# Kernel tuning notes

Measured on AMD Instinct MI355X. Metric: run time of the kernel, lower is better.

Reference implementation:

```python
import jax, jax.numpy as jnp
import numpy as np

B, L, D, E, K = 8, 384, 1024, 4, 2
H = 4 * D  # expert MLP hidden


def setup_inputs() -> dict:
    key = jax.random.key(0)
    ks = jax.random.split(key, 10)
    def w(k, shape, fan_in):
        return jax.random.normal(k, shape, jnp.float32) / np.sqrt(fan_in).astype(np.float32)
    return {
        "context_c": jax.random.normal(ks[0], (B, L, D), jnp.float32),
        "time_cond": jax.random.normal(ks[1], (B, D), jnp.float32),
        "gate_W": w(ks[2], (E, 3 * D), 3 * D),
        "gate_b": jnp.zeros((E,), jnp.float32),
        "tmod_W": w(ks[3], (2 * E, D), D),
        "tmod_b": jnp.zeros((2 * E,), jnp.float32),
        "eW1": w(ks[4], (E, D, H), D),
        "eb1": jnp.zeros((E, H), jnp.float32),
        "eW2": w(ks[5], (E, H, D), H),
        "eb2": jnp.zeros((E, D), jnp.float32),
        "sW1": w(ks[6], (D, H), D),
        "sb1": jnp.zeros((H,), jnp.float32),
        "sW2": w(ks[7], (H, D), H),
        "sb2": jnp.zeros((D,), jnp.float32),
    }


def reference(context_c, time_cond, gate_W, gate_b, tmod_W, tmod_b,
              eW1, eb1, eW2, eb2, sW1, sb1, sW2, sb2):
    Lh = Lw = L // 3
    Lp = L - Lh - Lw
    head = context_c[:, :Lh]            # (B, Lh, D)
    wrist = context_c[:, Lh:Lh + Lw]    # (B, Lw, D)
    prop = context_c[:, Lh + Lw:]       # (B, Lp, D)

    # per-sample modality-combo aggregates for the gate
    full_agg = context_c.mean(axis=1)
    hp_agg = (head.sum(axis=1) + prop.sum(axis=1)) / (Lh + Lp)
    wp_agg = (wrist.sum(axis=1) + prop.sum(axis=1)) / (Lw + Lp)
    gate_in = jnp.concatenate([full_agg, hp_agg, wp_agg], axis=-1)  # (B, 3D)

    logits = gate_in @ gate_W.T + gate_b                            # (B, E)
    mod = jax.nn.silu(time_cond) @ tmod_W.T + tmod_b                # (B, 2E)
    scale, shift = mod[:, :E], mod[:, E:]
    logits = logits * (1.0 + scale) + shift

    scores = jax.nn.softmax(logits, axis=-1)
    tw, ti = jax.lax.top_k(scores, K)                               # (B, K)
    tw = tw / (tw.sum(axis=-1, keepdims=True) + 1e-8)
    # per-sample combined weight for each expert: (B, E)
    w_be = (jax.nn.one_hot(ti, E, dtype=tw.dtype) * tw[..., None]).sum(axis=1)

    # modality mask per expert (E, L): expert 1 skips wrist, expert 2 skips head
    mask_np = np.ones((E, L), np.float32)
    mask_np[1, Lh:Lh + Lw] = 0.0
    mask_np[2, :Lh] = 0.0
    mask = jnp.asarray(mask_np)

    # run all experts on all tokens (token-wise MLP), combine with per-sample
    # routing weights and per-expert modality masks — identical math to the
    # original per-sample sliced dispatch.
    h = jax.nn.gelu(jnp.einsum('bld,edh->belh', context_c, eW1)
                    + eb1[None, :, None, :], approximate=True)      # (B,E,L,H)
    y = jnp.einsum('belh,ehd->beld', h, eW2) + eb2[None, :, None, :]
    out = jnp.einsum('be,el,beld->bld', w_be, mask, y)

    # shared expert (always-on)
    shared = jax.nn.gelu(context_c @ sW1 + sb1, approximate=True) @ sW2 + sb2
    return out + shared
```

## Files before the change

### kernel.cpp

```cpp
#include <hip/hip_runtime.h>
#include <cstdint>
#include <cstddef>


#define DEV __device__ __forceinline__

typedef __attribute__((ext_vector_type(8))) __bf16 bf16x8;
typedef __attribute__((ext_vector_type(4))) __bf16 bf16x4;
typedef __attribute__((ext_vector_type(4))) float f32x4;

static constexpr int Bb = 8, Ll = 384, Dd = 1024, Ee = 4, Hh = 4096;

DEV void load_lds16(const void* g, void* l) {
  __builtin_amdgcn_global_load_lds(
      (const __attribute__((address_space(1))) void*)g,
      (__attribute__((address_space(3))) void*)l, 16, 0, 0);
}

DEV float gelu_tanh(float x) {
  float u = 0.7978845608028654f * (x + 0.044715f * x * x * x);
  float t = 1.0f - 2.0f / (1.0f + __expf(2.0f * u));
  return 0.5f * x * (1.0f + t);
}

DEV float wave_red(float v) {
#pragma unroll
  for (int o = 32; o > 0; o >>= 1) v += __shfl_down(v, o, 64);
  return v;
}


__global__ void cvt_x_kernel(const float* __restrict__ src, __bf16* __restrict__ dst, int n4) {
  int i = blockIdx.x * blockDim.x + threadIdx.x;
  if (i >= n4) return;
  float4 v = ((const float4*)src)[i];
  bf16x4 o;
  o.x = (__bf16)v.x; o.y = (__bf16)v.y; o.z = (__bf16)v.z; o.w = (__bf16)v.w;
  ((bf16x4*)dst)[i] = o;
}

__global__ void transpose_cvt_kernel(const float* __restrict__ src, __bf16* __restrict__ dst,
                                     int nr, int nc) {
  __shared__ float t[32][33];
  size_t base = (size_t)blockIdx.z * nr * nc;
  src += base; dst += base;
  int x = threadIdx.x & 31, y = threadIdx.x >> 5;
  int c0 = blockIdx.x * 32, r0 = blockIdx.y * 32;
#pragma unroll
  for (int r = 0; r < 4; ++r) {
    int rr = y + r * 8;
    t[rr][x] = src[(size_t)(r0 + rr) * nc + c0 + x];
  }
  __syncthreads();
#pragma unroll
  for (int r = 0; r < 4; ++r) {
    int rr = y + r * 8;
    dst[(size_t)(c0 + rr) * nr + r0 + x] = (__bf16)t[x][rr];
  }
}


__global__ void agg_kernel(const float* __restrict__ ctx, float* __restrict__ part) {
  int c = blockIdx.x, b = blockIdx.y, t = threadIdx.x;
  int d0 = t * 4;
  float4 sum = {0.f, 0.f, 0.f, 0.f};
  const float* p = ctx + ((size_t)(b * Ll + c * 64)) * Dd + d0;
  for (int l = 0; l < 64; ++l) {
    float4 v = *(const float4*)(p + (size_t)l * Dd);
    sum.x += v.x; sum.y += v.y; sum.z += v.z; sum.w += v.w;
  }
  *(float4*)(part + ((size_t)(b * 6 + c)) * Dd + d0) = sum;
}

__global__ void gate_kernel(const float* __restrict__ part, const float* __restrict__ tc,
                            const float* __restrict__ gW, const float* __restrict__ gb,
                            const float* __restrict__ tW, const float* __restrict__ tb,
                            int* __restrict__ slotE, float* __restrict__ slotW) {
  __shared__ float gi[3 * Dd];
  __shared__ float st[Dd];
  __shared__ float red[12];
  int b = blockIdx.x, t = threadIdx.x;
  const float* pb = part + (size_t)b * 6 * Dd;
#pragma unroll
  for (int k = 0; k < 4; ++k) {
    int d = t * 4 + k;
    float p0 = pb[d], p1 = pb[Dd + d], p2 = pb[2 * Dd + d];
    float p3 = pb[3 * Dd + d], p4 = pb[4 * Dd + d], p5 = pb[5 * Dd + d];
    gi[d]          = (p0 + p1 + p2 + p3 + p4 + p5) * (1.0f / 384.0f);
    gi[Dd + d]     = (p0 + p1 + p4 + p5) * (1.0f / 256.0f);
    gi[2 * Dd + d] = (p2 + p3 + p4 + p5) * (1.0f / 256.0f);
    float tv = tc[b * Dd + d];
    st[d] = tv / (1.0f + __expf(-tv));
  }
  __syncthreads();
  int wid = t >> 6, lane = t & 63;
  float aL = 0.f;
  for (int i = lane; i < 3 * Dd; i += 64) aL += gi[i] * gW[wid * 3 * Dd + i];
  aL = wave_red(aL);
  float aA = 0.f, aB = 0.f;
  for (int i = lane; i < Dd; i += 64) {
    float s = st[i];
    aA += s * tW[wid * Dd + i];
    aB += s * tW[(wid + 4) * Dd + i];
  }
  aA = wave_red(aA); aB = wave_red(aB);
  if (lane == 0) { red[wid] = aL; red[4 + wid] = aA; red[8 + wid] = aB; }
  __syncthreads();
  if (t == 0) {
    float lg[4];
#pragma unroll
    for (int e = 0; e < 4; ++e) {
      float logit = red[e] + gb[e];
      float scale = red[4 + e] + tb[e];
      float shift = red[8 + e] + tb[4 + e];
      lg[e] = logit * (1.0f + scale) + shift;
    }
    float m = fmaxf(fmaxf(lg[0], lg[1]), fmaxf(lg[2], lg[3]));
    float p[4], sum = 0.f;
#pragma unroll
    for (int e = 0; e < 4; ++e) { p[e] = __expf(lg[e] - m); sum += p[e]; }
#pragma unroll
    for (int e = 0; e < 4; ++e) p[e] /= sum;
    int i0 = 0;
    for (int e = 1; e < 4; ++e) if (p[e] > p[i0]) i0 = e;
    int i1 = -1;
    for (int e = 0; e < 4; ++e) if (e != i0 && (i1 < 0 || p[e] > p[i1])) i1 = e;
    float sw = p[i0] + p[i1] + 1e-8f;
    slotE[b * 4 + 0] = i0; slotE[b * 4 + 1] = i1;
    slotW[b * 4 + 0] = p[i0] / sw; slotW[b * 4 + 1] = p[i1] / sw;
  }
}


__global__ __launch_bounds__(256) void gemm1_kernel(
    const __bf16* __restrict__ Xbf, const __bf16* __restrict__ W1T,
    const __bf16* __restrict__ S1T, const float* __restrict__ eb1,
    const float* __restrict__ sb1, const int* __restrict__ slotE,
    const float* __restrict__ slotW, __bf16* __restrict__ Hbuf, int bbase) {
  constexpr int K = Dd;
  int nt = blockIdx.x, mt = blockIdx.y, z = blockIdx.z;
  int bl = z / 3, s = z - bl * 3;
  int b = bbase + bl;
  int e = (s == 2) ? Ee : slotE[b * 4 + s];
  if ((e == 1 && mt == 1) || (e == 2 && mt == 0)) return;
  float wgt = (s == 2) ? 1.0f : slotW[b * 4 + s];

  const __bf16* Ab = Xbf + ((size_t)(b * Ll + mt * 128)) * K;
  const __bf16* Bbp = (e < Ee ? W1T + (size_t)e * Hh * K : S1T) + (size_t)(nt * 128) * K;
  const float* b1p = (e < Ee ? eb1 + e * Hh : sb1);

  __shared__ __align__(16) char smem[65536];

  int tid = threadIdx.x, wid = tid >> 6, lane = tid & 63;
  int q = lane >> 4, l16 = lane & 15;
  int wm = wid >> 1, wn = wid & 1;

  const __bf16* gp[8];
  uint32_t lo[8];
#pragma unroll
  for (int u = 0; u < 8; ++u) {
    int c = wid * 8 + u;
    int isB = c >> 4;
    int blk = (c & 15) >> 1;
    int ks = c & 1;
    const __bf16* base = isB ? Bbp : Ab;
    gp[u] = base + (size_t)(blk * 16 + l16) * K + ks * 32 + q * 8;
    lo[u] = (uint32_t)(isB * 16384 + (blk * 2 + ks) * 1024);
  }

  f32x4 acc[4][4];
  f32x4 zero = {0.f, 0.f, 0.f, 0.f};
#pragma unroll
  for (int i = 0; i < 4; ++i)
#pragma unroll
    for (int j = 0; j < 4; ++j) acc[i][j] = zero;

#pragma unroll
  for (int u = 0; u < 8; ++u) load_lds16(gp[u], smem + lo[u]);

  constexpr int NK = K / 64;
  for (int kt = 0; kt < NK; ++kt) {
    int ph = kt & 1;
    __syncthreads();
    if (kt + 1 < NK) {
#pragma unroll
      for (int u = 0; u < 8; ++u) {
        gp[u] += 64;
        load_lds16(gp[u], smem + lo[u] + (ph ^ 1) * 32768);
      }
    }
    const char* sm = (const char*)smem + ph * 32768;
#pragma unroll
    for (int ks = 0; ks < 2; ++ks) {
      bf16x8 a[4], bb[4];
#pragma unroll
      for (int i = 0; i < 4; ++i)
        a[i] = *(const bf16x8*)(sm + (((wm * 4 + i) * 2 + ks) * 64 + lane) * 16);
#pragma unroll
      for (int j = 0; j < 4; ++j)
        bb[j] = *(const bf16x8*)(sm + 16384 + (((wn * 4 + j) * 2 + ks) * 64 + lane) * 16);
#pragma unroll
      for (int i = 0; i < 4; ++i)
#pragma unroll
        for (int j = 0; j < 4; ++j)
          acc[i][j] = __builtin_amdgcn_mfma_f32_16x16x32_bf16(a[i], bb[j], acc[i][j], 0, 0, 0);
    }
  }

  float bias[4];
#pragma unroll
  for (int j = 0; j < 4; ++j) bias[j] = b1p[nt * 128 + wn * 64 + j * 16 + l16];

  __syncthreads();
  __bf16* tile = (__bf16*)smem;
#pragma unroll
  for (int i = 0; i < 4; ++i)
#pragma unroll
    for (int j = 0; j < 4; ++j)
#pragma unroll
      for (int r = 0; r < 4; ++r) {
        float x = acc[i][j][r] + bias[j];
        int row = wm * 64 + i * 16 + q * 4 + r;
        int col = wn * 64 + j * 16 + l16;
        tile[row * 136 + col] = (__bf16)(wgt * gelu_tanh(x));
      }
  __syncthreads();
  __bf16* Hrow = Hbuf + ((size_t)(bl * 3 + s) * Ll + mt * 128) * Hh + nt * 128;
#pragma unroll
  for (int t2 = 0; t2 < 8; ++t2) {
    int gidx = t2 * 256 + tid;
    int row = gidx >> 4, cg = gidx & 15;
    bf16x8 v = *(const bf16x8*)(tile + row * 136 + cg * 8);
    *(bf16x8*)(Hrow + (size_t)row * Hh + cg * 8) = v;
  }
}


__global__ __launch_bounds__(256) void gemm2_kernel(
    const __bf16* __restrict__ Hbuf, const __bf16* __restrict__ W2T,
    const __bf16* __restrict__ S2T, const float* __restrict__ eb2,
    const float* __restrict__ sb2, const int* __restrict__ slotE,
    const float* __restrict__ slotW, float* __restrict__ out,
    __bf16* __restrict__ pbuf, int bbase, int bc) {
  constexpr int K = Hh;
  constexpr int KC = 1024;
  int nt = blockIdx.x, mt = blockIdx.y, z = blockIdx.z;
  int kc = z & 3, bl = z >> 2;
  int b = bbase + bl;

  __shared__ __align__(16) char smem[65536];

  int tid = threadIdx.x, wid = tid >> 6, lane = tid & 63;
  int q = lane >> 4, l16 = lane & 15;
  int wm = wid >> 1, wn = wid & 1;

  f32x4 acc[4][4];
  f32x4 zero = {0.f, 0.f, 0.f, 0.f};
#pragma unroll
  for (int i = 0; i < 4; ++i)
#pragma unroll
    for (int j = 0; j < 4; ++j) acc[i][j] = zero;
  float biasacc[4] = {0.f, 0.f, 0.f, 0.f};

  for (int s = 0; s < 3; ++s) {
    int e = (s == 2) ? Ee : slotE[b * 4 + s];
    if ((e == 1 && mt == 1) || (e == 2 && mt == 0)) continue;
    float wgt = (s == 2) ? 1.0f : slotW[b * 4 + s];

    const __bf16* Ab = Hbuf + ((size_t)(bl * 3 + s) * Ll + mt * 128) * K + (size_t)kc * KC;
    const __bf16* Bbp = (e < Ee ? W2T + (size_t)e * Dd * K : S2T) + (size_t)(nt * 128) * K + (size_t)kc * KC;

    const __bf16* gp[8];
    uint32_t lo[8];
#pragma unroll
    for (int u = 0; u < 8; ++u) {
      int c = wid * 8 + u;
      int isB = c >> 4;
      int blk = (c & 15) >> 1;
      int ks = c & 1;
      const __bf16* base = isB ? Bbp : Ab;
      gp[u] = base + (size_t)(blk * 16 + l16) * K + ks * 32 + q * 8;
      lo[u] = (uint32_t)(isB * 16384 + (blk * 2 + ks) * 1024);
    }

#pragma unroll
    for (int u = 0; u < 8; ++u) load_lds16(gp[u], smem + lo[u]);

    constexpr int NK = KC / 64;
    for (int kt = 0; kt < NK; ++kt) {
      int ph = kt & 1;
      __syncthreads();
      if (kt + 1 < NK) {
#pragma unroll
        for (int u = 0; u < 8; ++u) {
          gp[u] += 64;
          load_lds16(gp[u], smem + lo[u] + (ph ^ 1) * 32768);
        }
      }
      const char* sm = (const char*)smem + ph * 32768;
#pragma unroll
      for (int ks = 0; ks < 2; ++ks) {
        bf16x8 a[4], bb[4];
#pragma unroll
        for (int i = 0; i < 4; ++i)
          a[i] = *(const bf16x8*)(sm + (((wm * 4 + i) * 2 + ks) * 64 + lane) * 16);
#pragma unroll
        for (int j = 0; j < 4; ++j)
          bb[j] = *(const bf16x8*)(sm + 16384 + (((wn * 4 + j) * 2 + ks) * 64 + lane) * 16);
#pragma unroll
        for (int i = 0; i < 4; ++i)
#pragma unroll
          for (int j = 0; j < 4; ++j)
            acc[i][j] = __builtin_amdgcn_mfma_f32_16x16x32_bf16(a[i], bb[j], acc[i][j], 0, 0, 0);
      }
    }

    if (kc == 0) {
      const float* b2p = (e < Ee ? eb2 + e * Dd : sb2);
#pragma unroll
      for (int j = 0; j < 4; ++j)
        biasacc[j] += wgt * b2p[nt * 128 + wn * 64 + j * 16 + l16];
    }
  }

  if (pbuf) {
    __syncthreads();
    __bf16* tile = (__bf16*)smem;
#pragma unroll
    for (int i = 0; i < 4; ++i)
#pragma unroll
      for (int j = 0; j < 4; ++j)
#pragma unroll
        for (int r = 0; r < 4; ++r) {
          int row = wm * 64 + i * 16 + q * 4 + r;
          int col = wn * 64 + j * 16 + l16;
          tile[row * 136 + col] = (__bf16)(acc[i][j][r] + biasacc[j]);
        }
    __syncthreads();
    __bf16* Prow = pbuf + (((size_t)(kc * bc + bl) * Ll + mt * 128)) * Dd + nt * 128;
#pragma unroll
    for (int t2 = 0; t2 < 8; ++t2) {
      int gidx = t2 * 256 + tid;
      int row = gidx >> 4, cg = gidx & 15;
      bf16x8 v = *(const bf16x8*)(tile + row * 136 + cg * 8);
      *(bf16x8*)(Prow + (size_t)row * Dd + cg * 8) = v;
    }
  } else {
    float* orow = out + ((size_t)(b * Ll + mt * 128)) * Dd + nt * 128;
#pragma unroll
    for (int i = 0; i < 4; ++i)
#pragma unroll
      for (int j = 0; j < 4; ++j)
#pragma unroll
        for (int r = 0; r < 4; ++r) {
          int row = wm * 64 + i * 16 + q * 4 + r;
          int col = wn * 64 + j * 16 + l16;
          atomicAdd(orow + (size_t)row * Dd + col, acc[i][j][r] + biasacc[j]);
        }
  }
}

__global__ void reduce4_kernel(const __bf16* __restrict__ pbuf, float* __restrict__ out,
                               int n8, size_t stride) {
  int i = blockIdx.x * blockDim.x + threadIdx.x;
  if (i >= n8) return;
  size_t base = (size_t)i * 8;
  float sum[8];
#pragma unroll
  for (int k = 0; k < 8; ++k) sum[k] = 0.f;
#pragma unroll
  for (int kc = 0; kc < 4; ++kc) {
    bf16x8 v = *(const bf16x8*)(pbuf + kc * stride + base);
#pragma unroll
    for (int k = 0; k < 8; ++k) sum[k] += (float)v[k];
  }
  float4 o0 = {sum[0], sum[1], sum[2], sum[3]};
  float4 o1 = {sum[4], sum[5], sum[6], sum[7]};
  *(float4*)(out + base) = o0;
  *(float4*)(out + base + 4) = o1;
}


extern "C" void kernel_launch(void* const* d_in, const int* in_sizes, int n_in,
                              void* d_out, int out_size, void* d_ws, size_t ws_size,
                              hipStream_t stream) {
  (void)in_sizes; (void)n_in;
  const float* ctx = (const float*)d_in[0];
  const float* tc  = (const float*)d_in[1];
  const float* gW  = (const float*)d_in[2];
  const float* gb  = (const float*)d_in[3];
  const float* tW  = (const float*)d_in[4];
  const float* tb  = (const float*)d_in[5];
  const float* eW1 = (const float*)d_in[6];
  const float* eb1 = (const float*)d_in[7];
  const float* eW2 = (const float*)d_in[8];
  const float* eb2 = (const float*)d_in[9];
  const float* sW1 = (const float*)d_in[10];
  const float* sb1 = (const float*)d_in[11];
  const float* sW2 = (const float*)d_in[12];
  const float* sb2 = (const float*)d_in[13];
  float* out = (float*)d_out;

  char* ws = (char*)d_ws;
  size_t off = 0;
  auto alloc = [&](size_t sz) { size_t o = off; off += (sz + 255) & ~(size_t)255; return o; };
  size_t oW1T = alloc((size_t)Ee * Hh * Dd * 2);
  size_t oW2T = alloc((size_t)Ee * Dd * Hh * 2);
  size_t oS1T = alloc((size_t)Hh * Dd * 2);
  size_t oS2T = alloc((size_t)Dd * Hh * 2);
  size_t oX   = alloc((size_t)Bb * Ll * Dd * 2);
  size_t oP   = alloc((size_t)Bb * 6 * Dd * 4);
  size_t oSE  = alloc(Bb * 4 * sizeof(int));
  size_t oSW  = alloc(Bb * 4 * sizeof(float));
  size_t fixed = off;

  auto hbufB = [&](int bc) { return (size_t)bc * 3 * Ll * Hh * 2; };
  auto pbufB = [&](int bc) { return (size_t)4 * bc * Ll * Dd * 2; };
  int bc = 1; bool use_pbuf = false;
  if (fixed + hbufB(8) + pbufB(8) + 512 <= ws_size)      { bc = 8; use_pbuf = true; }
  else if (fixed + hbufB(4) + pbufB(4) + 512 <= ws_size) { bc = 4; use_pbuf = true; }
  else if (fixed + hbufB(4) + 512 <= ws_size)            { bc = 4; use_pbuf = false; }
  else if (fixed + hbufB(2) + 512 <= ws_size)            { bc = 2; use_pbuf = false; }
  else                                                   { bc = 1; use_pbuf = false; }
  int nchunk = Bb / bc;
  size_t oH = alloc(hbufB(bc));
  size_t oPB = use_pbuf ? alloc(pbufB(bc)) : 0;

  __bf16* W1T = (__bf16*)(ws + oW1T);
  __bf16* W2T = (__bf16*)(ws + oW2T);
  __bf16* S1T = (__bf16*)(ws + oS1T);
  __bf16* S2T = (__bf16*)(ws + oS2T);
  __bf16* Xbf = (__bf16*)(ws + oX);
  float*  part = (float*)(ws + oP);
  int*    slotE = (int*)(ws + oSE);
  float*  slotW = (float*)(ws + oSW);
  __bf16* Hbuf = (__bf16*)(ws + oH);
  __bf16* Pbuf = use_pbuf ? (__bf16*)(ws + oPB) : nullptr;

  if (!use_pbuf)
    hipMemsetAsync(d_out, 0, (size_t)out_size * sizeof(float), stream);

  cvt_x_kernel<<<(Bb * Ll * Dd / 4 + 255) / 256, 256, 0, stream>>>(ctx, Xbf, Bb * Ll * Dd / 4);
  transpose_cvt_kernel<<<dim3(Hh / 32, Dd / 32, Ee), 256, 0, stream>>>(eW1, W1T, Dd, Hh);
  transpose_cvt_kernel<<<dim3(Dd / 32, Hh / 32, Ee), 256, 0, stream>>>(eW2, W2T, Hh, Dd);
  transpose_cvt_kernel<<<dim3(Hh / 32, Dd / 32, 1), 256, 0, stream>>>(sW1, S1T, Dd, Hh);
  transpose_cvt_kernel<<<dim3(Dd / 32, Hh / 32, 1), 256, 0, stream>>>(sW2, S2T, Hh, Dd);
  agg_kernel<<<dim3(6, Bb), 256, 0, stream>>>(ctx, part);
  gate_kernel<<<Bb, 256, 0, stream>>>(part, tc, gW, gb, tW, tb, slotE, slotW);

  for (int c = 0; c < nchunk; ++c) {
    gemm1_kernel<<<dim3(Hh / 128, 3, bc * 3), 256, 0, stream>>>(
        Xbf, W1T, S1T, eb1, sb1, slotE, slotW, Hbuf, c * bc);
    gemm2_kernel<<<dim3(Dd / 128, 3, bc * 4), 256, 0, stream>>>(
        Hbuf, W2T, S2T, eb2, sb2, slotE, slotW, out, Pbuf, c * bc, bc);
    if (use_pbuf) {
      int n8 = bc * Ll * Dd / 8;
      reduce4_kernel<<<(n8 + 255) / 256, 256, 0, stream>>>(
          Pbuf, out + (size_t)c * bc * Ll * Dd, n8, (size_t)bc * Ll * Dd);
    }
  }
}
```

Baseline: 581.3 us.

## Remap GEMM workgroups XCD-aware and deepen gemm2 split-K to eight chunks

Both GEMM kernels switch to a flat 1D grid and remap block IDs so consecutive logical tiles land on the same XCD (bid&7 striding). This is meant to improve L2 reuse of weight and activation tiles across the MI355X chiplets. gemm2 is templated on its K-chunk size and, when workspace allows, uses 8 K-chunks of 512 instead of 4 of 1024, doubling the block count to fill more CUs. The cost is a larger partial buffer and more reduction traffic in the generalized reduce kernel.

```diff
diff --git a/kernel.cpp b/kernel.cpp
--- a/kernel.cpp
+++ b/kernel.cpp
@@ -138,8 +138,13 @@
     const float* __restrict__ sb1, const int* __restrict__ slotE,
     const float* __restrict__ slotW, __bf16* __restrict__ Hbuf, int bbase) {
   constexpr int K = Dd;
-  int nt = blockIdx.x, mt = blockIdx.y, z = blockIdx.z;
-  int bl = z / 3, s = z - bl * 3;
+  int bid = blockIdx.x, nwg = gridDim.x;
+  int lid = (bid & 7) * (nwg >> 3) + (bid >> 3);
+  int nt = lid & 31;
+  int r = lid >> 5;
+  int mt = r % 3; r /= 3;
+  int s = r % 3;
+  int bl = r / 3;
   int b = bbase + bl;
   int e = (s == 2) ? Ee : slotE[b * 4 + s];
   if ((e == 1 && mt == 1) || (e == 2 && mt == 0)) return;
@@ -218,9 +223,9 @@
 #pragma unroll
     for (int j = 0; j < 4; ++j)
 #pragma unroll
-      for (int r = 0; r < 4; ++r) {
-        float x = acc[i][j][r] + bias[j];
-        int row = wm * 64 + i * 16 + q * 4 + r;
+      for (int r2 = 0; r2 < 4; ++r2) {
+        float x = acc[i][j][r2] + bias[j];
+        int row = wm * 64 + i * 16 + q * 4 + r2;
         int col = wn * 64 + j * 16 + l16;
         tile[row * 136 + col] = (__bf16)(wgt * gelu_tanh(x));
       }
@@ -236,6 +241,7 @@
 }
 
 
+template <int KC>
 __global__ __launch_bounds__(256) void gemm2_kernel(
     const __bf16* __restrict__ Hbuf, const __bf16* __restrict__ W2T,
     const __bf16* __restrict__ S2T, const float* __restrict__ eb2,
@@ -243,9 +249,14 @@
     const float* __restrict__ slotW, float* __restrict__ out,
     __bf16* __restrict__ pbuf, int bbase, int bc) {
   constexpr int K = Hh;
-  constexpr int KC = 1024;
-  int nt = blockIdx.x, mt = blockIdx.y, z = blockIdx.z;
-  int kc = z & 3, bl = z >> 2;
+  constexpr int NKC = Hh / KC;
+  int bid = blockIdx.x, nwg = gridDim.x;
+  int lid = (bid & 7) * (nwg >> 3) + (bid >> 3);
+  int nt = lid & 7;
+  int r = lid >> 3;
+  int mt = r % 3; r /= 3;
+  int kc = r % NKC;
+  int bl = r / NKC;
   int b = bbase + bl;
 
   __shared__ __align__(16) char smem[65536];
@@ -331,10 +342,10 @@
 #pragma unroll
       for (int j = 0; j < 4; ++j)
 #pragma unroll
-        for (int r = 0; r < 4; ++r) {
-          int row = wm * 64 + i * 16 + q * 4 + r;
+        for (int r2 = 0; r2 < 4; ++r2) {
+          int row = wm * 64 + i * 16 + q * 4 + r2;
           int col = wn * 64 + j * 16 + l16;
-          tile[row * 136 + col] = (__bf16)(acc[i][j][r] + biasacc[j]);
+          tile[row * 136 + col] = (__bf16)(acc[i][j][r2] + biasacc[j]);
         }
     __syncthreads();
     __bf16* Prow = pbuf + (((size_t)(kc * bc + bl) * Ll + mt * 128)) * Dd + nt * 128;
@@ -352,24 +363,23 @@
 #pragma unroll
       for (int j = 0; j < 4; ++j)
 #pragma unroll
-        for (int r = 0; r < 4; ++r) {
-          int row = wm * 64 + i * 16 + q * 4 + r;
+        for (int r2 = 0; r2 < 4; ++r2) {
+          int row = wm * 64 + i * 16 + q * 4 + r2;
           int col = wn * 64 + j * 16 + l16;
-          atomicAdd(orow + (size_t)row * Dd + col, acc[i][j][r] + biasacc[j]);
+          atomicAdd(orow + (size_t)row * Dd + col, acc[i][j][r2] + biasacc[j]);
         }
   }
 }
 
-__global__ void reduce4_kernel(const __bf16* __restrict__ pbuf, float* __restrict__ out,
-                               int n8, size_t stride) {
+__global__ void reduce_kernel(const __bf16* __restrict__ pbuf, float* __restrict__ out,
+                              int n8, size_t stride, int nkc) {
   int i = blockIdx.x * blockDim.x + threadIdx.x;
   if (i >= n8) return;
   size_t base = (size_t)i * 8;
   float sum[8];
 #pragma unroll
   for (int k = 0; k < 8; ++k) sum[k] = 0.f;
-#pragma unroll
-  for (int kc = 0; kc < 4; ++kc) {
+  for (int kc = 0; kc < nkc; ++kc) {
     bf16x8 v = *(const bf16x8*)(pbuf + kc * stride + base);
 #pragma unroll
     for (int k = 0; k < 8; ++k) sum[k] += (float)v[k];
@@ -415,16 +425,17 @@
   size_t fixed = off;
 
   auto hbufB = [&](int bc) { return (size_t)bc * 3 * Ll * Hh * 2; };
-  auto pbufB = [&](int bc) { return (size_t)4 * bc * Ll * Dd * 2; };
-  int bc = 1; bool use_pbuf = false;
-  if (fixed + hbufB(8) + pbufB(8) + 512 <= ws_size)      { bc = 8; use_pbuf = true; }
-  else if (fixed + hbufB(4) + pbufB(4) + 512 <= ws_size) { bc = 4; use_pbuf = true; }
-  else if (fixed + hbufB(4) + 512 <= ws_size)            { bc = 4; use_pbuf = false; }
-  else if (fixed + hbufB(2) + 512 <= ws_size)            { bc = 2; use_pbuf = false; }
-  else                                                   { bc = 1; use_pbuf = false; }
+  auto pbufB = [&](int bc, int nkc) { return (size_t)nkc * bc * Ll * Dd * 2; };
+  int bc = 1; bool use_pbuf = false; int nkc = 4;
+  if (fixed + hbufB(8) + pbufB(8, 8) + 512 <= ws_size)      { bc = 8; use_pbuf = true; nkc = 8; }
+  else if (fixed + hbufB(8) + pbufB(8, 4) + 512 <= ws_size) { bc = 8; use_pbuf = true; nkc = 4; }
+  else if (fixed + hbufB(4) + pbufB(4, 4) + 512 <= ws_size) { bc = 4; use_pbuf = true; nkc = 4; }
+  else if (fixed + hbufB(4) + 512 <= ws_size)               { bc = 4; use_pbuf = false; nkc = 4; }
+  else if (fixed + hbufB(2) + 512 <= ws_size)               { bc = 2; use_pbuf = false; nkc = 4; }
+  else                                                      { bc = 1; use_pbuf = false; nkc = 4; }
   int nchunk = Bb / bc;
   size_t oH = alloc(hbufB(bc));
-  size_t oPB = use_pbuf ? alloc(pbufB(bc)) : 0;
+  size_t oPB = use_pbuf ? alloc(pbufB(bc, nkc)) : 0;
 
   __bf16* W1T = (__bf16*)(ws + oW1T);
   __bf16* W2T = (__bf16*)(ws + oW2T);
@@ -449,14 +460,19 @@
   gate_kernel<<<Bb, 256, 0, stream>>>(part, tc, gW, gb, tW, tb, slotE, slotW);
 
   for (int c = 0; c < nchunk; ++c) {
-    gemm1_kernel<<<dim3(Hh / 128, 3, bc * 3), 256, 0, stream>>>(
+    gemm1_kernel<<<dim3(288 * bc), 256, 0, stream>>>(
         Xbf, W1T, S1T, eb1, sb1, slotE, slotW, Hbuf, c * bc);
-    gemm2_kernel<<<dim3(Dd / 128, 3, bc * 4), 256, 0, stream>>>(
-        Hbuf, W2T, S2T, eb2, sb2, slotE, slotW, out, Pbuf, c * bc, bc);
+    int g2 = 8 * 3 * nkc * bc;
+    if (nkc == 8)
+      gemm2_kernel<512><<<dim3(g2), 256, 0, stream>>>(
+          Hbuf, W2T, S2T, eb2, sb2, slotE, slotW, out, Pbuf, c * bc, bc);
+    else
+      gemm2_kernel<1024><<<dim3(g2), 256, 0, stream>>>(
+          Hbuf, W2T, S2T, eb2, sb2, slotE, slotW, out, Pbuf, c * bc, bc);
     if (use_pbuf) {
       int n8 = bc * Ll * Dd / 8;
-      reduce4_kernel<<<(n8 + 255) / 256, 256, 0, stream>>>(
-          Pbuf, out + (size_t)c * bc * Ll * Dd, n8, (size_t)bc * Ll * Dd);
-    }
-  }
-}
+      reduce_kernel<<<(n8 + 255) / 256, 256, 0, stream>>>(
+          Pbuf, out + (size_t)c * bc * Ll * Dd, n8, (size_t)bc * Ll * Dd, nkc);
+    }
+  }
+}
```

After: 563.2 us. -3.1%, faster.
